# Optimization experiments

Measured on AMD Instinct MI355X. Metric: run time of the kernel, lower is better.

Reference implementation:

```python
import jax, jax.numpy as jnp
import numpy as np

M = 2_000_000   # total messages
N = 100_000     # unique destination nodes (segments)
D = 128         # message_dim


def setup_inputs() -> dict:
    key = jax.random.key(0)
    k1, k2, k3, k4 = jax.random.split(key, 4)
    msgs = jax.random.normal(k1, (M, D), dtype=jnp.float32)
    seg_ids = jnp.sort(jax.random.randint(k2, (M,), 0, N))
    timestamps = jax.random.randint(k3, (M,), 0, 1_000_000, dtype=jnp.int32)
    # scorer: nn.Linear(D, 1) -> weight vector [D] and scalar bias
    W = jax.random.normal(k4, (D,), dtype=jnp.float32) * (1.0 / np.sqrt(D))
    b = jnp.zeros((), dtype=jnp.float32)
    return {"msgs": msgs, "seg_ids": seg_ids, "timestamps": timestamps,
            "W": W, "b": b, "num_segments": N}


def reference(msgs, seg_ids, timestamps, W, b, num_segments):
    # per-message score: Linear(D, 1).squeeze(-1)
    scores = msgs @ W + b                                   # [M]
    # numerically-stable segment softmax over messages of each node
    seg_max = jax.ops.segment_max(scores, seg_ids, num_segments=num_segments)  # [N]
    e = jnp.exp(scores - seg_max[seg_ids])                  # [M]
    denom = jax.ops.segment_sum(e, seg_ids, num_segments=num_segments)         # [N]
    weights = e / denom[seg_ids]                            # [M]
    # weighted scatter-add: aggregated[n] = sum_i w_i * msg_i over segment n
    aggregated = jax.ops.segment_sum(weights[:, None] * msgs, seg_ids,
                                     num_segments=num_segments)  # [N, D]
    # original returns the LAST timestamp per node; ids are sorted and
    # timestamps within a node list are time-ordered, so last == max
    ts = jax.ops.segment_max(timestamps, seg_ids, num_segments=num_segments)   # [N]
    return aggregated, ts
```

## Files before the change

kernel.cpp:

```cpp
#include <hip/hip_runtime.h>
#include <cstdint>
#include <cstddef>

#define WAVES_PER_BLOCK 4

__global__ __launch_bounds__(256) void seg_bounds_kernel(
    const int* __restrict__ seg_ids, int* __restrict__ seg_start, int M, int N) {
    int i = blockIdx.x * blockDim.x + threadIdx.x;
    if (i >= M) return;
    int cur  = seg_ids[i];
    int prev = (i == 0) ? -1 : seg_ids[i - 1];
    for (int n = prev + 1; n <= cur; ++n) seg_start[n] = i;
    if (i == M - 1) {
        for (int n = cur + 1; n <= N; ++n) seg_start[n] = M;
    }
}

__global__ __launch_bounds__(256) void seg_softmax_agg_kernel(
    const float2* __restrict__ msgs2,
    const int*    __restrict__ timestamps,
    const float2* __restrict__ W2,
    const float*  __restrict__ b_ptr,
    const int*    __restrict__ seg_start,
    float2*       __restrict__ out_agg2,
    float*        __restrict__ out_ts,
    int N) {
    const int wave = threadIdx.x >> 6;
    const int lane = threadIdx.x & 63;
    const int n = blockIdx.x * WAVES_PER_BLOCK + wave;
    if (n >= N) return;

    const int s = seg_start[n];
    const int e = seg_start[n + 1];

    const float2 w2 = W2[lane];
    const float  bb = b_ptr[0];

    float2 acc  = make_float2(0.0f, 0.0f);
    float  mrun = -INFINITY;
    float  denom = 0.0f;
    int    tsm  = (-2147483647 - 1);

    if (e > s) {
        float2 mv = msgs2[(size_t)s * 64 + lane];
        int    tv = timestamps[s];
        for (int j = s; j < e; ++j) {
            float2 mv_cur = mv;
            int    tv_cur = tv;
            if (j + 1 < e) {
                mv = msgs2[(size_t)(j + 1) * 64 + lane];
                tv = timestamps[j + 1];
            }
            float part = mv_cur.x * w2.x + mv_cur.y * w2.y;
            #pragma unroll
            for (int off = 32; off >= 1; off >>= 1)
                part += __shfl_xor(part, off);
            const float sc = part + bb;

            const float mnew  = fmaxf(mrun, sc);
            const float alpha = __expf(mrun - mnew);
            const float wgt   = __expf(sc - mnew);
            denom = denom * alpha + wgt;
            acc.x = acc.x * alpha + wgt * mv_cur.x;
            acc.y = acc.y * alpha + wgt * mv_cur.y;
            tsm   = (tv_cur > tsm) ? tv_cur : tsm;
            mrun  = mnew;
        }
    }

    const float inv = (e > s) ? (1.0f / denom) : 0.0f;
    float2 o;
    o.x = acc.x * inv;
    o.y = acc.y * inv;
    out_agg2[(size_t)n * 64 + lane] = o;
    if (lane == 0) {
        out_ts[n] = (e > s) ? (float)tsm : -2147483648.0f;
    }
}

extern "C" void kernel_launch(void* const* d_in, const int* in_sizes, int n_in,
                              void* d_out, int out_size, void* d_ws, size_t ws_size,
                              hipStream_t stream) {
    const float* msgs       = (const float*)d_in[0];
    const int*   seg_ids    = (const int*)d_in[1];
    const int*   timestamps = (const int*)d_in[2];
    const float* W          = (const float*)d_in[3];
    const float* b          = (const float*)d_in[4];

    const int M = in_sizes[1];
    const int N = out_size / 129;

    int* seg_start = (int*)d_ws;

    float* out_agg = (float*)d_out;
    float* out_ts  = (float*)d_out + (size_t)N * 128;

    seg_bounds_kernel<<<(M + 255) / 256, 256, 0, stream>>>(seg_ids, seg_start, M, N);

    const int blocks = (N + WAVES_PER_BLOCK - 1) / WAVES_PER_BLOCK;
    seg_softmax_agg_kernel<<<blocks, 256, 0, stream>>>(
        (const float2*)msgs, timestamps, (const float2*)W, b, seg_start,
        (float2*)out_agg, out_ts, N);
}
```

Baseline: 1.358 ms.

## Process eight messages per wave step with float4 half-wave rows

```diff
diff --git a/kernel.cpp b/kernel.cpp
--- a/kernel.cpp
+++ b/kernel.cpp
@@ -1,6 +1,7 @@
 #include <hip/hip_runtime.h>
 #include <cstdint>
 #include <cstddef>
+#include <climits>
 
 #define WAVES_PER_BLOCK 4
 
@@ -17,62 +18,125 @@
 }
 
 __global__ __launch_bounds__(256) void seg_softmax_agg_kernel(
-    const float2* __restrict__ msgs2,
+    const float4* __restrict__ msgs4,
     const int*    __restrict__ timestamps,
-    const float2* __restrict__ W2,
+    const float4* __restrict__ W4,
     const float*  __restrict__ b_ptr,
     const int*    __restrict__ seg_start,
-    float2*       __restrict__ out_agg2,
+    float4*       __restrict__ out_agg4,
     float*        __restrict__ out_ts,
-    int N) {
+    int N, int M) {
     const int wave = threadIdx.x >> 6;
     const int lane = threadIdx.x & 63;
+    const int half = lane >> 5;
+    const int li   = lane & 31;
     const int n = blockIdx.x * WAVES_PER_BLOCK + wave;
     if (n >= N) return;
 
     const int s = seg_start[n];
     const int e = seg_start[n + 1];
 
-    const float2 w2 = W2[lane];
+    const float4 w4 = W4[li];
     const float  bb = b_ptr[0];
 
-    float2 acc  = make_float2(0.0f, 0.0f);
+    int tsm = INT_MIN;
+    for (int j = s + lane; j < e; j += 64) {
+        int tv = timestamps[j];
+        tsm = (tv > tsm) ? tv : tsm;
+    }
+    #pragma unroll
+    for (int off = 32; off >= 1; off >>= 1) {
+        int o = __shfl_xor(tsm, off);
+        tsm = (o > tsm) ? o : tsm;
+    }
+
+    float4 acc  = make_float4(0.f, 0.f, 0.f, 0.f);
     float  mrun = -INFINITY;
-    float  denom = 0.0f;
-    int    tsm  = (-2147483647 - 1);
+    float  denom = 0.f;
 
     if (e > s) {
-        float2 mv = msgs2[(size_t)s * 64 + lane];
-        int    tv = timestamps[s];
-        for (int j = s; j < e; ++j) {
-            float2 mv_cur = mv;
-            int    tv_cur = tv;
-            if (j + 1 < e) {
-                mv = msgs2[(size_t)(j + 1) * 64 + lane];
-                tv = timestamps[j + 1];
+        float4 nx0, nx1, nx2, nx3;
+        nx0 = msgs4[(size_t)min(s + 0 + half, M - 1) * 32 + li];
+        nx1 = msgs4[(size_t)min(s + 2 + half, M - 1) * 32 + li];
+        nx2 = msgs4[(size_t)min(s + 4 + half, M - 1) * 32 + li];
+        nx3 = msgs4[(size_t)min(s + 6 + half, M - 1) * 32 + li];
+
+        for (int j = s; j < e; j += 8) {
+            const float4 c0 = nx0, c1 = nx1, c2 = nx2, c3 = nx3;
+            const int jn = j + 8;
+            if (jn < e) {
+                nx0 = msgs4[(size_t)min(jn + 0 + half, M - 1) * 32 + li];
+                nx1 = msgs4[(size_t)min(jn + 2 + half, M - 1) * 32 + li];
+                nx2 = msgs4[(size_t)min(jn + 4 + half, M - 1) * 32 + li];
+                nx3 = msgs4[(size_t)min(jn + 6 + half, M - 1) * 32 + li];
             }
-            float part = mv_cur.x * w2.x + mv_cur.y * w2.y;
+
+            float p0 = c0.x * w4.x + c0.y * w4.y + c0.z * w4.z + c0.w * w4.w;
+            float p1 = c1.x * w4.x + c1.y * w4.y + c1.z * w4.z + c1.w * w4.w;
+            float p2 = c2.x * w4.x + c2.y * w4.y + c2.z * w4.z + c2.w * w4.w;
+            float p3 = c3.x * w4.x + c3.y * w4.y + c3.z * w4.z + c3.w * w4.w;
+
             #pragma unroll
-            for (int off = 32; off >= 1; off >>= 1)
-                part += __shfl_xor(part, off);
-            const float sc = part + bb;
+            for (int off = 16; off >= 1; off >>= 1) {
+                p0 += __shfl_xor(p0, off);
+                p1 += __shfl_xor(p1, off);
+                p2 += __shfl_xor(p2, off);
+                p3 += __shfl_xor(p3, off);
+            }
+            const float q0 = __shfl_xor(p0, 32);
+            const float q1 = __shfl_xor(p1, 32);
+            const float q2 = __shfl_xor(p2, 32);
+            const float q3 = __shfl_xor(p3, 32);
 
-            const float mnew  = fmaxf(mrun, sc);
+            const float NEG = -INFINITY;
+            const float s0 = (j + 0 < e) ? ((half ? q0 : p0) + bb) : NEG;
+            const float s1 = (j + 1 < e) ? ((half ? p0 : q0) + bb) : NEG;
+            const float s2 = (j + 2 < e) ? ((half ? q1 : p1) + bb) : NEG;
+            const float s3 = (j + 3 < e) ? ((half ? p1 : q1) + bb) : NEG;
+            const float s4 = (j + 4 < e) ? ((half ? q2 : p2) + bb) : NEG;
+            const float s5 = (j + 5 < e) ? ((half ? p2 : q2) + bb) : NEG;
+            const float s6 = (j + 6 < e) ? ((half ? q3 : p3) + bb) : NEG;
+            const float s7 = (j + 7 < e) ? ((half ? p3 : q3) + bb) : NEG;
+
+            const float mc = fmaxf(fmaxf(fmaxf(s0, s1), fmaxf(s2, s3)),
+                                   fmaxf(fmaxf(s4, s5), fmaxf(s6, s7)));
+            const float mnew  = fmaxf(mrun, mc);
             const float alpha = __expf(mrun - mnew);
-            const float wgt   = __expf(sc - mnew);
-            denom = denom * alpha + wgt;
-            acc.x = acc.x * alpha + wgt * mv_cur.x;
-            acc.y = acc.y * alpha + wgt * mv_cur.y;
-            tsm   = (tv_cur > tsm) ? tv_cur : tsm;
-            mrun  = mnew;
+            const float w0 = __expf(s0 - mnew);
+            const float w1 = __expf(s1 - mnew);
+            const float w2 = __expf(s2 - mnew);
+            const float w3 = __expf(s3 - mnew);
+            const float w4w = __expf(s4 - mnew);
+            const float w5 = __expf(s5 - mnew);
+            const float w6 = __expf(s6 - mnew);
+            const float w7 = __expf(s7 - mnew);
+
+            denom = denom * alpha + (((w0 + w1) + (w2 + w3)) + ((w4w + w5) + (w6 + w7)));
+
+            const float wl0 = half ? w1 : w0;
+            const float wl1 = half ? w3 : w2;
+            const float wl2 = half ? w5 : w4w;
+            const float wl3 = half ? w7 : w6;
+
+            acc.x = acc.x * alpha + wl0 * c0.x + wl1 * c1.x + wl2 * c2.x + wl3 * c3.x;
+            acc.y = acc.y * alpha + wl0 * c0.y + wl1 * c1.y + wl2 * c2.y + wl3 * c3.y;
+            acc.z = acc.z * alpha + wl0 * c0.z + wl1 * c1.z + wl2 * c2.z + wl3 * c3.z;
+            acc.w = acc.w * alpha + wl0 * c0.w + wl1 * c1.w + wl2 * c2.w + wl3 * c3.w;
+
+            mrun = mnew;
         }
     }
 
+    acc.x += __shfl_xor(acc.x, 32);
+    acc.y += __shfl_xor(acc.y, 32);
+    acc.z += __shfl_xor(acc.z, 32);
+    acc.w += __shfl_xor(acc.w, 32);
+
     const float inv = (e > s) ? (1.0f / denom) : 0.0f;
-    float2 o;
-    o.x = acc.x * inv;
-    o.y = acc.y * inv;
-    out_agg2[(size_t)n * 64 + lane] = o;
+    if (lane < 32) {
+        out_agg4[(size_t)n * 32 + lane] =
+            make_float4(acc.x * inv, acc.y * inv, acc.z * inv, acc.w * inv);
+    }
     if (lane == 0) {
         out_ts[n] = (e > s) ? (float)tsm : -2147483648.0f;
     }
@@ -99,6 +163,6 @@
 
     const int blocks = (N + WAVES_PER_BLOCK - 1) / WAVES_PER_BLOCK;
     seg_softmax_agg_kernel<<<blocks, 256, 0, stream>>>(
-        (const float2*)msgs, timestamps, (const float2*)W, b, seg_start,
-        (float2*)out_agg, out_ts, N);
+        (const float4*)msgs, timestamps, (const float4*)W, b, seg_start,
+        (float4*)out_agg, out_ts, N, M);
 }
```

After: 1.298 ms. 1.05x faster.
